# Optimization experiments

Measured on AMD Instinct MI355X. Metric: run time of the kernel, lower is better.

The kernel has to match this reference:

```python
import jax, jax.numpy as jnp
import numpy as np

B, T, I, D = 64, 1024, 64, 256  # batch, seq_len, input_size, hidden_size


def setup_inputs() -> dict:
    key = jax.random.key(0)
    ks = jax.random.split(key, 9)
    s = 0.05  # small init scale for numerical stability
    return {
        "x": jax.random.normal(ks[0], (B, T, I), dtype=jnp.float32),
        "W_ih": jax.random.normal(ks[1], (4 * D, I), dtype=jnp.float32) * s,
        "W_hh": jax.random.normal(ks[2], (4 * D, D), dtype=jnp.float32) * s,
        "b_ih": jax.random.normal(ks[3], (4 * D,), dtype=jnp.float32) * s,
        "b_hh": jax.random.normal(ks[4], (4 * D,), dtype=jnp.float32) * s,
        "W1": jax.random.normal(ks[5], (D, 2 * D), dtype=jnp.float32) * s,
        "b1": jax.random.normal(ks[6], (D,), dtype=jnp.float32) * s,
        "W2": jax.random.normal(ks[7], (I, D), dtype=jnp.float32) * s,
        "b2": jax.random.normal(ks[8], (I,), dtype=jnp.float32) * s,
    }


def _lstm_scan(x, W_ih, W_hh, b_ih, b_hh):
    # x: [B, T, I] -> hidden states H: [B, T, D]
    xT = jnp.swapaxes(x, 0, 1)  # [T, B, I]
    h0 = jnp.zeros((x.shape[0], D), dtype=x.dtype)
    c0 = jnp.zeros((x.shape[0], D), dtype=x.dtype)

    def step(carry, x_t):
        h, c = carry
        gates = x_t @ W_ih.T + b_ih + h @ W_hh.T + b_hh  # [B, 4D]
        i_g, f_g, g_g, o_g = jnp.split(gates, 4, axis=-1)  # torch LSTMCell gate order
        c = jax.nn.sigmoid(f_g) * c + jax.nn.sigmoid(i_g) * jnp.tanh(g_g)
        h = jax.nn.sigmoid(o_g) * jnp.tanh(c)
        return (h, c), h

    _, H = jax.lax.scan(step, (h0, c0), xT)
    return jnp.swapaxes(H, 0, 1)  # [B, T, D]


def reference(x, W_ih, W_hh, b_ih, b_hh, W1, b1, W2, b2):
    # Eval mode: dropout is identity.
    H = _lstm_scan(x, W_ih, W_hh, b_ih, b_hh)  # [B, T, D]
    # Per-step attention over all past (incl. current) hidden states == unscaled
    # causal self-attention with Q=K=V=H.
    scores = jnp.einsum("btd,bsd->bts", H, H)  # [B, T, T]
    t_idx = jnp.arange(H.shape[1])
    causal = t_idx[None, :] <= t_idx[:, None]  # key s <= query t
    scores = jnp.where(causal[None], scores, -jnp.inf)
    weights = jax.nn.softmax(scores, axis=-1)
    context = jnp.einsum("bts,bsd->btd", weights, H)  # [B, T, D]
    combined = jnp.concatenate([H, context], axis=-1)  # [B, T, 2D]
    hid = jax.nn.relu(combined @ W1.T + b1)  # [B, T, D]
    return hid @ W2.T + b2  # [B, T, I]
```

## Files before the change

### kernel.cpp

```cpp
#include <hip/hip_runtime.h>
#include <hip/hip_bf16.h>

#define Bn 64
#define Tn 1024
#define In 64
#define Dn 256

typedef short bf16x8 __attribute__((ext_vector_type(8)));
typedef unsigned short u16x8 __attribute__((ext_vector_type(8)));
typedef unsigned short u16x4 __attribute__((ext_vector_type(4)));
typedef float f32x4 __attribute__((ext_vector_type(4)));
typedef unsigned int u32x2 __attribute__((ext_vector_type(2)));

__device__ __forceinline__ unsigned short f2bf(float f){
  unsigned u = __float_as_uint(f);
  u += 0x7fffu + ((u >> 16) & 1u);
  return (unsigned short)(u >> 16);
}
__device__ __forceinline__ float sig_(float x){ return 1.f / (1.f + __expf(-x)); }
__device__ __forceinline__ float tanh_(float x){ float e = __expf(2.f * x); return 1.f - 2.f / (e + 1.f); }

__device__ __forceinline__ bf16x8 pack8(const float* f){
  bf16x8 r;
  #pragma unroll
  for (int i = 0; i < 8; ++i) r[i] = (short)f2bf(f[i]);
  return r;
}

__global__ __launch_bounds__(256, 1) void gates_x_kernel(
    const float* __restrict__ x, const float* __restrict__ Wih,
    const float* __restrict__ bih, const float* __restrict__ bhh,
    unsigned short* __restrict__ Gx)
{
  const int bid = blockIdx.x;
  const int chain = bid >> 8;
  const int t0 = (bid & 255) * 4;
  const int tid = threadIdx.x;
  const int wv = tid >> 6;
  const int l = tid & 63;
  const int lr = l & 15, lg = l >> 4;
  const int gate = lr & 3, dimx = lr >> 2;

  __shared__ float bsum[1024];
  for (int r = tid; r < 1024; r += 256) bsum[r] = bih[r] + bhh[r];
  __syncthreads();

  bf16x8 wa[16][2];
  #pragma unroll
  for (int up = 0; up < 2; ++up)
    #pragma unroll
    for (int j = 0; j < 2; ++j)
      #pragma unroll
      for (int mt = 0; mt < 4; ++mt){
        const int u = wv * 2 + up;
        const int row = gate * Dn + u * 32 + j * 16 + dimx * 4 + mt;
        #pragma unroll
        for (int kt = 0; kt < 2; ++kt){
          float tmp[8];
          *(float4*)&tmp[0] = *(const float4*)&Wih[row * In + kt * 32 + lg * 8];
          *(float4*)&tmp[4] = *(const float4*)&Wih[row * In + kt * 32 + lg * 8 + 4];
          wa[(up * 2 + j) * 4 + mt][kt] = pack8(tmp);
        }
      }

  const int b = chain * 16 + lr;
  for (int tt = 0; tt < 4; ++tt){
    const int t = t0 + tt;
    bf16x8 xb[2];
    #pragma unroll
    for (int kt = 0; kt < 2; ++kt){
      float tmp[8];
      *(float4*)&tmp[0] = *(const float4*)&x[(size_t)(b * Tn + t) * In + kt * 32 + lg * 8];
      *(float4*)&tmp[4] = *(const float4*)&x[(size_t)(b * Tn + t) * In + kt * 32 + lg * 8 + 4];
      xb[kt] = pack8(tmp);
    }
    #pragma unroll
    for (int up = 0; up < 2; ++up)
      #pragma unroll
      for (int j = 0; j < 2; ++j)
        #pragma unroll
        for (int mt = 0; mt < 4; ++mt){
          const int u = wv * 2 + up;
          f32x4 a = {0.f, 0.f, 0.f, 0.f};
          a = __builtin_amdgcn_mfma_f32_16x16x32_bf16(wa[(up*2+j)*4+mt][0], xb[0], a, 0, 0, 0);
          a = __builtin_amdgcn_mfma_f32_16x16x32_bf16(wa[(up*2+j)*4+mt][1], xb[1], a, 0, 0, 0);
          const int dim = u * 32 + j * 16 + lg * 4 + mt;
          u16x4 o;
          #pragma unroll
          for (int i = 0; i < 4; ++i) o[i] = f2bf(a[i] + bsum[i * Dn + dim]);
          const size_t off = (((size_t)(chain * Tn + t) * 8 + u) * 8 + (j * 4 + mt)) * 256
                             + (lg * 16 + lr) * 4;
          *(u16x4*)&Gx[off] = o;
        }
  }
}

__global__ __launch_bounds__(512, 1) void lstm_scan_kernel(
    const unsigned short* __restrict__ Gx, const float* __restrict__ Whh,
    unsigned short* __restrict__ Hbf)
{
  const int chain = blockIdx.x;
  const int tid = threadIdx.x;
  const int u = tid >> 6;
  const int l = tid & 63;
  const int lr = l & 15, lg = l >> 4;
  const int gate = lr & 3, dimx = lr >> 2;

  __shared__ unsigned short WL[8][18 * 512];
  __shared__ unsigned short hL[32][16][8];

  bf16x8 w0[4][8], w1m0[8], w1m3h[6];
  #pragma unroll
  for (int mt = 0; mt < 4; ++mt){
    const int row = gate * Dn + u * 32 + dimx * 4 + mt;
    #pragma unroll
    for (int kt = 0; kt < 8; ++kt){
      float tmp[8];
      *(float4*)&tmp[0] = *(const float4*)&Whh[row * Dn + kt * 32 + lg * 8];
      *(float4*)&tmp[4] = *(const float4*)&Whh[row * Dn + kt * 32 + lg * 8 + 4];
      w0[mt][kt] = pack8(tmp);
    }
  }
  {
    const int row = gate * Dn + u * 32 + 16 + dimx * 4 + 0;
    #pragma unroll
    for (int kt = 0; kt < 8; ++kt){
      float tmp[8];
      *(float4*)&tmp[0] = *(const float4*)&Whh[row * Dn + kt * 32 + lg * 8];
      *(float4*)&tmp[4] = *(const float4*)&Whh[row * Dn + kt * 32 + lg * 8 + 4];
      w1m0[kt] = pack8(tmp);
    }
  }
  {
    const int row = gate * Dn + u * 32 + 16 + dimx * 4 + 3;
    #pragma unroll
    for (int kt = 2; kt < 8; ++kt){
      float tmp[8];
      *(float4*)&tmp[0] = *(const float4*)&Whh[row * Dn + kt * 32 + lg * 8];
      *(float4*)&tmp[4] = *(const float4*)&Whh[row * Dn + kt * 32 + lg * 8 + 4];
      w1m3h[kt - 2] = pack8(tmp);
    }
  }
  #pragma unroll
  for (int mt = 1; mt < 3; ++mt){
    const int row = gate * Dn + u * 32 + 16 + dimx * 4 + mt;
    #pragma unroll
    for (int kt = 0; kt < 8; ++kt){
      float tmp[8];
      *(float4*)&tmp[0] = *(const float4*)&Whh[row * Dn + kt * 32 + lg * 8];
      *(float4*)&tmp[4] = *(const float4*)&Whh[row * Dn + kt * 32 + lg * 8 + 4];
      *(bf16x8*)&WL[u][((mt - 1) * 8 + kt) * 512 + lg * 128 + lr * 8] = pack8(tmp);
    }
  }
  {
    const int row = gate * Dn + u * 32 + 16 + dimx * 4 + 3;
    #pragma unroll
    for (int kt = 0; kt < 2; ++kt){
      float tmp[8];
      *(float4*)&tmp[0] = *(const float4*)&Whh[row * Dn + kt * 32 + lg * 8];
      *(float4*)&tmp[4] = *(const float4*)&Whh[row * Dn + kt * 32 + lg * 8 + 4];
      *(bf16x8*)&WL[u][(16 + kt) * 512 + lg * 128 + lr * 8] = pack8(tmp);
    }
  }
  for (int i = tid; i < 32 * 16 * 8; i += 512) ((unsigned short*)hL)[i] = 0;
  __syncthreads();

  float cst[8] = {0.f, 0.f, 0.f, 0.f, 0.f, 0.f, 0.f, 0.f};
  const int lane64 = lg * 16 + lr;

  u32x2 g[8];
  {
    const unsigned short* gxp = Gx + ((size_t)(chain * Tn + 0) * 8 + u) * 2048;
    #pragma unroll
    for (int jm = 0; jm < 8; ++jm)
      g[jm] = *(const u32x2*)&gxp[jm * 256 + lane64 * 4];
  }

  const size_t hbB = (size_t)(chain * 16 + lr) * Tn * Dn;

  for (int t = 0; t < Tn; ++t){
    f32x4 acc[8];
    #pragma unroll
    for (int i = 0; i < 8; ++i) acc[i] = (f32x4){0.f, 0.f, 0.f, 0.f};

    #pragma unroll
    for (int kt = 0; kt < 8; ++kt){
      const bf16x8 hf = *(const bf16x8*)&hL[kt * 4 + lg][lr][0];
      acc[0] = __builtin_amdgcn_mfma_f32_16x16x32_bf16(w0[0][kt], hf, acc[0], 0, 0, 0);
      acc[1] = __builtin_amdgcn_mfma_f32_16x16x32_bf16(w0[1][kt], hf, acc[1], 0, 0, 0);
      acc[2] = __builtin_amdgcn_mfma_f32_16x16x32_bf16(w0[2][kt], hf, acc[2], 0, 0, 0);
      acc[3] = __builtin_amdgcn_mfma_f32_16x16x32_bf16(w0[3][kt], hf, acc[3], 0, 0, 0);
      acc[4] = __builtin_amdgcn_mfma_f32_16x16x32_bf16(w1m0[kt], hf, acc[4], 0, 0, 0);
      acc[5] = __builtin_amdgcn_mfma_f32_16x16x32_bf16(
                 *(const bf16x8*)&WL[u][(0 * 8 + kt) * 512 + lg * 128 + lr * 8], hf, acc[5], 0, 0, 0);
      acc[6] = __builtin_amdgcn_mfma_f32_16x16x32_bf16(
                 *(const bf16x8*)&WL[u][(1 * 8 + kt) * 512 + lg * 128 + lr * 8], hf, acc[6], 0, 0, 0);
      bf16x8 a7;
      if (kt < 2) a7 = *(const bf16x8*)&WL[u][(16 + kt) * 512 + lg * 128 + lr * 8];
      else        a7 = w1m3h[kt - 2];
      acc[7] = __builtin_amdgcn_mfma_f32_16x16x32_bf16(a7, hf, acc[7], 0, 0, 0);
    }
    __syncthreads();

    unsigned long long hq0 = 0, hq1 = 0;
    #pragma unroll
    for (int jm = 0; jm < 8; ++jm){
      const int mt = jm & 3;
      const unsigned glo = g[jm][0], ghi = g[jm][1];
      const float gi = __uint_as_float(glo << 16)         + acc[jm][0];
      const float gf = __uint_as_float(glo & 0xFFFF0000u) + acc[jm][1];
      const float gg = __uint_as_float(ghi << 16)         + acc[jm][2];
      const float go = __uint_as_float(ghi & 0xFFFF0000u) + acc[jm][3];
      const float ig = sig_(gi), fg = sig_(gf), gv = tanh_(gg), og = sig_(go);
      const float c = fg * cst[jm] + ig * gv;
      cst[jm] = c;
      const float h = og * tanh_(c);
      const unsigned long long hb = (unsigned long long)f2bf(h) << (16 * mt);
      if (jm < 4) hq0 |= hb; else hq1 |= hb;
    }
    {
      const int db0 = u * 4 + (lg >> 1);
      *(unsigned long long*)&hL[db0][lr][(lg & 1) * 4]     = hq0;
      *(unsigned long long*)&hL[db0 + 2][lr][(lg & 1) * 4] = hq1;
    }
    {
      const size_t o = hbB + (size_t)t * Dn + u * 32 + lg * 4;
      *(unsigned long long*)&Hbf[o]      = hq0;
      *(unsigned long long*)&Hbf[o + 16] = hq1;
    }
    {
      const int tn = (t + 1 < Tn) ? t + 1 : t;
      const unsigned short* gxp = Gx + ((size_t)(chain * Tn + tn) * 8 + u) * 2048;
      #pragma unroll
      for (int jm = 0; jm < 8; ++jm)
        g[jm] = *(const u32x2*)&gxp[jm * 256 + lane64 * 4];
    }
    __syncthreads();
  }
}

__global__ __launch_bounds__(256, 1) void attn_kernel(
    const unsigned short* __restrict__ Hbf, unsigned short* __restrict__ ctxbf)
{
  const int bid = blockIdx.x;
  const int b = bid >> 4, qt = bid & 15;
  const int q0 = qt * 64;
  const int tid = threadIdx.x;
  const int w = tid >> 6, l = tid & 63;
  const int lr = l & 15, lg = l >> 4;

  __shared__ unsigned short Qs[64 * 256];
  __shared__ unsigned short Ks[64 * 256];
  __shared__ unsigned short Vt[256 * 64];
  __shared__ unsigned short Ps[64 * 64];

  {
    const int r = tid >> 2, cs = (tid & 3) * 64;
    #pragma unroll
    for (int jj = 0; jj < 8; ++jj){
      const int c = cs + jj * 8;
      u16x8 v = *(const u16x8*)&Hbf[(b * Tn + q0 + r) * Dn + c];
      *(u16x8*)((char*)Qs + (((r * 256 + c) * 2) ^ ((r & 7) << 4))) = v;
    }
  }
  __syncthreads();
  bf16x8 qf[8];
  #pragma unroll
  for (int kc = 0; kc < 8; ++kc){
    const int r = w * 16 + lr, c = kc * 32 + lg * 8;
    qf[kc] = *(const bf16x8*)((const char*)Qs + (((r * 256 + c) * 2) ^ ((r & 7) << 4)));
  }

  float m_i[4], l_i[4];
  f32x4 o_acc[16];
  #pragma unroll
  for (int i = 0; i < 4; ++i){ m_i[i] = -__builtin_inff(); l_i[i] = 0.f; }
  #pragma unroll
  for (int n = 0; n < 16; ++n) o_acc[n] = (f32x4){0.f, 0.f, 0.f, 0.f};

  for (int kt = 0; kt <= qt; ++kt){
    const int s0 = kt * 64;
    __syncthreads();
    {
      const int r = tid >> 2, cs = (tid & 3) * 64;
      #pragma unroll
      for (int jj = 0; jj < 8; ++jj){
        const int c = cs + jj * 8;
        u16x8 v = *(const u16x8*)&Hbf[(b * Tn + s0 + r) * Dn + c];
        *(u16x8*)((char*)Ks + (((r * 256 + c) * 2) ^ ((r & 7) << 4))) = v;
      }
    }
    {
      const int s = tid & 63, db = tid >> 6;
      #pragma unroll
      for (int jj = 0; jj < 8; ++jj){
        const int d0 = db * 64 + jj * 8;
        u16x8 v = *(const u16x8*)&Hbf[(b * Tn + s0 + s) * Dn + d0];
        #pragma unroll
        for (int e = 0; e < 8; ++e){
          const int d = d0 + e;
          *(unsigned short*)((char*)Vt + (((d * 64 + s) * 2) ^ ((d & 7) << 4))) = (unsigned short)v[e];
        }
      }
    }
    __syncthreads();
    f32x4 sacc[4];
    #pragma unroll
    for (int n = 0; n < 4; ++n) sacc[n] = (f32x4){0.f, 0.f, 0.f, 0.f};
    #pragma unroll
    for (int kc = 0; kc < 8; ++kc){
      #pragma unroll
      for (int n = 0; n < 4; ++n){
        const int r = n * 16 + lr, c = kc * 32 + lg * 8;
        bf16x8 kfr = *(const bf16x8*)((const char*)Ks + (((r * 256 + c) * 2) ^ ((r & 7) << 4)));
        sacc[n] = __builtin_amdgcn_mfma_f32_16x16x32_bf16(qf[kc], kfr, sacc[n], 0, 0, 0);
      }
    }
    if (kt == qt){
      #pragma unroll
      for (int n = 0; n < 4; ++n)
        #pragma unroll
        for (int i = 0; i < 4; ++i){
          const int scol = s0 + n * 16 + lr;
          const int qrow = q0 + w * 16 + lg * 4 + i;
          if (scol > qrow) sacc[n][i] = -__builtin_inff();
        }
    }
    float rmax[4], alpha[4], rsum[4];
    #pragma unroll
    for (int i = 0; i < 4; ++i){
      float vv = fmaxf(fmaxf(sacc[0][i], sacc[1][i]), fmaxf(sacc[2][i], sacc[3][i]));
      vv = fmaxf(vv, __shfl_xor(vv, 1));
      vv = fmaxf(vv, __shfl_xor(vv, 2));
      vv = fmaxf(vv, __shfl_xor(vv, 4));
      vv = fmaxf(vv, __shfl_xor(vv, 8));
      rmax[i] = vv;
    }
    #pragma unroll
    for (int i = 0; i < 4; ++i){
      const float mn = fmaxf(m_i[i], rmax[i]);
      alpha[i] = __expf(m_i[i] - mn);
      m_i[i] = mn;
      rsum[i] = 0.f;
    }
    #pragma unroll
    for (int n = 0; n < 4; ++n){
      #pragma unroll
      for (int i = 0; i < 4; ++i){
        const float pv = __expf(sacc[n][i] - m_i[i]);
        rsum[i] += pv;
        const int r = w * 16 + lg * 4 + i, c = n * 16 + lr;
        *(unsigned short*)((char*)Ps + (((r * 64 + c) * 2) ^ ((r & 7) << 4))) = f2bf(pv);
      }
    }
    #pragma unroll
    for (int i = 0; i < 4; ++i){
      float vv = rsum[i];
      vv += __shfl_xor(vv, 1);
      vv += __shfl_xor(vv, 2);
      vv += __shfl_xor(vv, 4);
      vv += __shfl_xor(vv, 8);
      l_i[i] = l_i[i] * alpha[i] + vv;
    }
    #pragma unroll
    for (int n = 0; n < 16; ++n)
      #pragma unroll
      for (int i = 0; i < 4; ++i) o_acc[n][i] *= alpha[i];
    #pragma unroll
    for (int kc = 0; kc < 2; ++kc){
      const int r = w * 16 + lr, c = kc * 32 + lg * 8;
      bf16x8 pfr = *(const bf16x8*)((const char*)Ps + (((r * 64 + c) * 2) ^ ((r & 7) << 4)));
      #pragma unroll
      for (int n = 0; n < 16; ++n){
        const int vr = n * 16 + lr, vc = kc * 32 + lg * 8;
        bf16x8 vfr = *(const bf16x8*)((const char*)Vt + (((vr * 64 + vc) * 2) ^ ((vr & 7) << 4)));
        o_acc[n] = __builtin_amdgcn_mfma_f32_16x16x32_bf16(pfr, vfr, o_acc[n], 0, 0, 0);
      }
    }
  }
  #pragma unroll
  for (int n = 0; n < 16; ++n)
    #pragma unroll
    for (int i = 0; i < 4; ++i){
      const float vv = o_acc[n][i] / l_i[i];
      const int q = q0 + w * 16 + lg * 4 + i;
      const int d = n * 16 + lr;
      ctxbf[(b * Tn + q) * Dn + d] = f2bf(vv);
    }
}

__global__ __launch_bounds__(256, 1) void mlp_kernel(
    const unsigned short* __restrict__ Hbf, const unsigned short* __restrict__ ctxbf,
    const float* __restrict__ W1, const float* __restrict__ b1,
    const float* __restrict__ W2, const float* __restrict__ b2,
    float* __restrict__ out)
{
  const int m0 = blockIdx.x * 64;
  const int tid = threadIdx.x;
  const int w = tid >> 6, l = tid & 63;
  const int lr = l & 15, lg = l >> 4;

  __shared__ unsigned short As[64 * 512];
  __shared__ unsigned short Ws[64 * 512];

  {
    const int r = tid >> 2, cs = (tid & 3) * 128;
    #pragma unroll
    for (int jj = 0; jj < 16; ++jj){
      const int c = cs + jj * 8;
      u16x8 v;
      if (c < 256) v = *(const u16x8*)&Hbf[(m0 + r) * Dn + c];
      else         v = *(const u16x8*)&ctxbf[(m0 + r) * Dn + (c - 256)];
      *(u16x8*)((char*)As + (((r * 512 + c) * 2) ^ ((r & 7) << 4))) = v;
    }
  }
  f32x4 hacc[16];
  #pragma unroll
  for (int n = 0; n < 16; ++n) hacc[n] = (f32x4){0.f, 0.f, 0.f, 0.f};

  for (int nb = 0; nb < 4; ++nb){
    __syncthreads();
    {
      const int r = tid >> 2, cs = (tid & 3) * 128;
      #pragma unroll
      for (int jj = 0; jj < 32; ++jj){
        const int c = cs + jj * 4;
        const float4 v = *(const float4*)&W1[(nb * 64 + r) * 512 + c];
        u16x4 pk = { f2bf(v.x), f2bf(v.y), f2bf(v.z), f2bf(v.w) };
        *(u16x4*)((char*)Ws + (((r * 512 + c) * 2) ^ ((r & 7) << 4))) = pk;
      }
    }
    __syncthreads();
    #pragma unroll
    for (int kc = 0; kc < 16; ++kc){
      const int ar = w * 16 + lr, ac = kc * 32 + lg * 8;
      bf16x8 af = *(const bf16x8*)((const char*)As + (((ar * 512 + ac) * 2) ^ ((ar & 7) << 4)));
      #pragma unroll
      for (int n = 0; n < 4; ++n){
        const int br = n * 16 + lr;
        bf16x8 bf = *(const bf16x8*)((const char*)Ws + (((br * 512 + ac) * 2) ^ ((br & 7) << 4)));
        hacc[nb * 4 + n] = __builtin_amdgcn_mfma_f32_16x16x32_bf16(af, bf, hacc[nb * 4 + n], 0, 0, 0);
      }
    }
  }
  __syncthreads();
  #pragma unroll
  for (int nn = 0; nn < 16; ++nn){
    const int col = (nn >> 2) * 64 + (nn & 3) * 16 + lr;
    const float bv = b1[col];
    #pragma unroll
    for (int i = 0; i < 4; ++i){
      float v = hacc[nn][i] + bv;
      v = v > 0.f ? v : 0.f;
      const int r = w * 16 + lg * 4 + i;
      *(unsigned short*)((char*)As + (((r * 256 + col) * 2) ^ ((r & 7) << 4))) = f2bf(v);
    }
  }
  {
    const int r = tid >> 2, cs = (tid & 3) * 64;
    #pragma unroll
    for (int jj = 0; jj < 16; ++jj){
      const int c = cs + jj * 4;
      const float4 v = *(const float4*)&W2[r * 256 + c];
      u16x4 pk = { f2bf(v.x), f2bf(v.y), f2bf(v.z), f2bf(v.w) };
      *(u16x4*)((char*)Ws + (((r * 256 + c) * 2) ^ ((r & 7) << 4))) = pk;
    }
  }
  __syncthreads();
  f32x4 oacc[4];
  #pragma unroll
  for (int n = 0; n < 4; ++n) oacc[n] = (f32x4){0.f, 0.f, 0.f, 0.f};
  #pragma unroll
  for (int kc = 0; kc < 8; ++kc){
    const int ar = w * 16 + lr, ac = kc * 32 + lg * 8;
    bf16x8 af = *(const bf16x8*)((const char*)As + (((ar * 256 + ac) * 2) ^ ((ar & 7) << 4)));
    #pragma unroll
    for (int n = 0; n < 4; ++n){
      const int br = n * 16 + lr;
      bf16x8 bf = *(const bf16x8*)((const char*)Ws + (((br * 256 + ac) * 2) ^ ((br & 7) << 4)));
      oacc[n] = __builtin_amdgcn_mfma_f32_16x16x32_bf16(af, bf, oacc[n], 0, 0, 0);
    }
  }
  #pragma unroll
  for (int n = 0; n < 4; ++n)
    #pragma unroll
    for (int i = 0; i < 4; ++i){
      const int ii = n * 16 + lr;
      const int m = m0 + w * 16 + lg * 4 + i;
      out[m * In + ii] = oacc[n][i] + b2[ii];
    }
}

extern "C" void kernel_launch(void* const* d_in, const int* in_sizes, int n_in,
                              void* d_out, int out_size, void* d_ws, size_t ws_size,
                              hipStream_t stream)
{
  (void)in_sizes; (void)n_in; (void)out_size; (void)ws_size;
  const float* x   = (const float*)d_in[0];
  const float* Wih = (const float*)d_in[1];
  const float* Whh = (const float*)d_in[2];
  const float* bih = (const float*)d_in[3];
  const float* bhh = (const float*)d_in[4];
  const float* W1  = (const float*)d_in[5];
  const float* b1  = (const float*)d_in[6];
  const float* W2  = (const float*)d_in[7];
  const float* b2  = (const float*)d_in[8];
  float* out = (float*)d_out;

  char* ws = (char*)d_ws;
  unsigned short* Hbf   = (unsigned short*)ws;
  unsigned short* ctxbf = (unsigned short*)(ws + (size_t)32 * 1024 * 1024);
  unsigned short* Gx    = (unsigned short*)(ws + (size_t)32 * 1024 * 1024);

  gates_x_kernel<<<1024, 256, 0, stream>>>(x, Wih, bih, bhh, Gx);
  lstm_scan_kernel<<<4, 512, 0, stream>>>(Gx, Whh, Hbf);
  attn_kernel<<<Bn * 16, 256, 0, stream>>>(Hbf, ctxbf);
  mlp_kernel<<<(Bn * Tn) / 64, 256, 0, stream>>>(Hbf, ctxbf, W1, b1, W2, b2, out);
}
```

Before: 5.039 ms.

## Double-buffer LSTM hidden state and split gate halves to drop a barrier

The recurrent hidden-state buffer in LDS is now double-buffered by step parity, which removes one of the two block-wide barriers in each time step. The eight gate tiles are split into two halves, so each half's elementwise LSTM update and h store can start while the other half's MFMAs are pending. The next-step Gx prefetch is replaced by loads issued inside the current step, which may leave global-load latency exposed. The launch attribute now pins waves-per-EU to 2, which tightens the register budget for the register-resident weights and could cause spills.

After: 4.144 ms. -17.8%, faster.

```diff
diff --git a/kernel.cpp b/kernel.cpp
--- a/kernel.cpp
+++ b/kernel.cpp
@@ -95,7 +95,9 @@
   }
 }
 
-__global__ __launch_bounds__(512, 1) void lstm_scan_kernel(
+__global__ void __attribute__((amdgpu_flat_work_group_size(512, 512),
+                               amdgpu_waves_per_eu(2, 2)))
+lstm_scan_kernel(
     const unsigned short* __restrict__ Gx, const float* __restrict__ Whh,
     unsigned short* __restrict__ Hbf)
 {
@@ -107,7 +109,7 @@
   const int gate = lr & 3, dimx = lr >> 2;
 
   __shared__ unsigned short WL[8][18 * 512];
-  __shared__ unsigned short hL[32][16][8];
+  __shared__ unsigned short hL[2][32][16][8];
 
   bf16x8 w0[4][8], w1m0[8], w1m3h[6];
   #pragma unroll
@@ -162,78 +164,91 @@
       *(bf16x8*)&WL[u][(16 + kt) * 512 + lg * 128 + lr * 8] = pack8(tmp);
     }
   }
-  for (int i = tid; i < 32 * 16 * 8; i += 512) ((unsigned short*)hL)[i] = 0;
+  for (int i = tid; i < 2 * 32 * 16 * 8; i += 512) ((unsigned short*)hL)[i] = 0;
   __syncthreads();
 
   float cst[8] = {0.f, 0.f, 0.f, 0.f, 0.f, 0.f, 0.f, 0.f};
   const int lane64 = lg * 16 + lr;
-
-  u32x2 g[8];
-  {
-    const unsigned short* gxp = Gx + ((size_t)(chain * Tn + 0) * 8 + u) * 2048;
-    #pragma unroll
-    for (int jm = 0; jm < 8; ++jm)
-      g[jm] = *(const u32x2*)&gxp[jm * 256 + lane64 * 4];
-  }
-
   const size_t hbB = (size_t)(chain * 16 + lr) * Tn * Dn;
+  const int db0 = u * 4 + (lg >> 1);
+  const int hoff = (lg & 1) * 4;
 
   for (int t = 0; t < Tn; ++t){
-    f32x4 acc[8];
-    #pragma unroll
-    for (int i = 0; i < 8; ++i) acc[i] = (f32x4){0.f, 0.f, 0.f, 0.f};
-
+    const int p = t & 1;
+    const unsigned short* gxp = Gx + ((size_t)(chain * Tn + t) * 8 + u) * 2048;
+
+    u32x2 gA[4];
+    #pragma unroll
+    for (int jm = 0; jm < 4; ++jm)
+      gA[jm] = *(const u32x2*)&gxp[jm * 256 + lane64 * 4];
+
+    f32x4 acc[4];
+    #pragma unroll
+    for (int i = 0; i < 4; ++i) acc[i] = (f32x4){0.f, 0.f, 0.f, 0.f};
     #pragma unroll
     for (int kt = 0; kt < 8; ++kt){
-      const bf16x8 hf = *(const bf16x8*)&hL[kt * 4 + lg][lr][0];
+      const bf16x8 hf = *(const bf16x8*)&hL[p][kt * 4 + lg][lr][0];
       acc[0] = __builtin_amdgcn_mfma_f32_16x16x32_bf16(w0[0][kt], hf, acc[0], 0, 0, 0);
       acc[1] = __builtin_amdgcn_mfma_f32_16x16x32_bf16(w0[1][kt], hf, acc[1], 0, 0, 0);
       acc[2] = __builtin_amdgcn_mfma_f32_16x16x32_bf16(w0[2][kt], hf, acc[2], 0, 0, 0);
       acc[3] = __builtin_amdgcn_mfma_f32_16x16x32_bf16(w0[3][kt], hf, acc[3], 0, 0, 0);
-      acc[4] = __builtin_amdgcn_mfma_f32_16x16x32_bf16(w1m0[kt], hf, acc[4], 0, 0, 0);
-      acc[5] = __builtin_amdgcn_mfma_f32_16x16x32_bf16(
-                 *(const bf16x8*)&WL[u][(0 * 8 + kt) * 512 + lg * 128 + lr * 8], hf, acc[5], 0, 0, 0);
-      acc[6] = __builtin_amdgcn_mfma_f32_16x16x32_bf16(
-                 *(const bf16x8*)&WL[u][(1 * 8 + kt) * 512 + lg * 128 + lr * 8], hf, acc[6], 0, 0, 0);
+    }
+    {
+      unsigned long long hq0 = 0;
+      #pragma unroll
+      for (int mt = 0; mt < 4; ++mt){
+        const unsigned glo = gA[mt][0], ghi = gA[mt][1];
+        const float gi = __uint_as_float(glo << 16)         + acc[mt][0];
+        const float gf = __uint_as_float(glo & 0xFFFF0000u) + acc[mt][1];
+        const float gg = __uint_as_float(ghi << 16)         + acc[mt][2];
+        const float go = __uint_as_float(ghi & 0xFFFF0000u) + acc[mt][3];
+        const float ig = sig_(gi), fg = sig_(gf), gv = tanh_(gg), og = sig_(go);
+        const float c = fg * cst[mt] + ig * gv;
+        cst[mt] = c;
+        const float h = og * tanh_(c);
+        hq0 |= (unsigned long long)f2bf(h) << (16 * mt);
+      }
+      *(unsigned long long*)&hL[p ^ 1][db0][lr][hoff] = hq0;
+      *(unsigned long long*)&Hbf[hbB + (size_t)t * Dn + u * 32 + lg * 4] = hq0;
+    }
+
+    u32x2 gB[4];
+    #pragma unroll
+    for (int jm = 0; jm < 4; ++jm)
+      gB[jm] = *(const u32x2*)&gxp[(4 + jm) * 256 + lane64 * 4];
+
+    #pragma unroll
+    for (int i = 0; i < 4; ++i) acc[i] = (f32x4){0.f, 0.f, 0.f, 0.f};
+    #pragma unroll
+    for (int kt = 0; kt < 8; ++kt){
+      const bf16x8 hf = *(const bf16x8*)&hL[p][kt * 4 + lg][lr][0];
+      acc[0] = __builtin_amdgcn_mfma_f32_16x16x32_bf16(w1m0[kt], hf, acc[0], 0, 0, 0);
+      acc[1] = __builtin_amdgcn_mfma_f32_16x16x32_bf16(
+                 *(const bf16x8*)&WL[u][(0 * 8 + kt) * 512 + lg * 128 + lr * 8], hf, acc[1], 0, 0, 0);
+      acc[2] = __builtin_amdgcn_mfma_f32_16x16x32_bf16(
+                 *(const bf16x8*)&WL[u][(1 * 8 + kt) * 512 + lg * 128 + lr * 8], hf, acc[2], 0, 0, 0);
       bf16x8 a7;
       if (kt < 2) a7 = *(const bf16x8*)&WL[u][(16 + kt) * 512 + lg * 128 + lr * 8];
       else        a7 = w1m3h[kt - 2];
-      acc[7] = __builtin_amdgcn_mfma_f32_16x16x32_bf16(a7, hf, acc[7], 0, 0, 0);
-    }
-    __syncthreads();
-
-    unsigned long long hq0 = 0, hq1 = 0;
-    #pragma unroll
-    for (int jm = 0; jm < 8; ++jm){
-      const int mt = jm & 3;
-      const unsigned glo = g[jm][0], ghi = g[jm][1];
-      const float gi = __uint_as_float(glo << 16)         + acc[jm][0];
-      const float gf = __uint_as_float(glo & 0xFFFF0000u) + acc[jm][1];
-      const float gg = __uint_as_float(ghi << 16)         + acc[jm][2];
-      const float go = __uint_as_float(ghi & 0xFFFF0000u) + acc[jm][3];
-      const float ig = sig_(gi), fg = sig_(gf), gv = tanh_(gg), og = sig_(go);
-      const float c = fg * cst[jm] + ig * gv;
-      cst[jm] = c;
-      const float h = og * tanh_(c);
-      const unsigned long long hb = (unsigned long long)f2bf(h) << (16 * mt);
-      if (jm < 4) hq0 |= hb; else hq1 |= hb;
+      acc[3] = __builtin_amdgcn_mfma_f32_16x16x32_bf16(a7, hf, acc[3], 0, 0, 0);
     }
     {
-      const int db0 = u * 4 + (lg >> 1);
-      *(unsigned long long*)&hL[db0][lr][(lg & 1) * 4]     = hq0;
-      *(unsigned long long*)&hL[db0 + 2][lr][(lg & 1) * 4] = hq1;
-    }
-    {
-      const size_t o = hbB + (size_t)t * Dn + u * 32 + lg * 4;
-      *(unsigned long long*)&Hbf[o]      = hq0;
-      *(unsigned long long*)&Hbf[o + 16] = hq1;
-    }
-    {
-      const int tn = (t + 1 < Tn) ? t + 1 : t;
-      const unsigned short* gxp = Gx + ((size_t)(chain * Tn + tn) * 8 + u) * 2048;
-      #pragma unroll
-      for (int jm = 0; jm < 8; ++jm)
-        g[jm] = *(const u32x2*)&gxp[jm * 256 + lane64 * 4];
+      unsigned long long hq1 = 0;
+      #pragma unroll
+      for (int mt = 0; mt < 4; ++mt){
+        const unsigned glo = gB[mt][0], ghi = gB[mt][1];
+        const float gi = __uint_as_float(glo << 16)         + acc[mt][0];
+        const float gf = __uint_as_float(glo & 0xFFFF0000u) + acc[mt][1];
+        const float gg = __uint_as_float(ghi << 16)         + acc[mt][2];
+        const float go = __uint_as_float(ghi & 0xFFFF0000u) + acc[mt][3];
+        const float ig = sig_(gi), fg = sig_(gf), gv = tanh_(gg), og = sig_(go);
+        const float c = fg * cst[4 + mt] + ig * gv;
+        cst[4 + mt] = c;
+        const float h = og * tanh_(c);
+        hq1 |= (unsigned long long)f2bf(h) << (16 * mt);
+      }
+      *(unsigned long long*)&hL[p ^ 1][db0 + 2][lr][hoff] = hq1;
+      *(unsigned long long*)&Hbf[hbB + (size_t)t * Dn + u * 32 + 16 + lg * 4] = hq1;
     }
     __syncthreads();
   }
```
